# Kernel tuning notes

Measured on AMD Instinct MI355X. Metric: run time of the kernel, lower is better.

The kernel has to match this reference:

```python
import jax, jax.numpy as jnp
import numpy as np

B, S, V, H, NL, NH, FF, L = 32, 256, 30522, 768, 12, 12, 3072, 9
DH = H // NH
SCALE = 1.0 / float(np.sqrt(DH))

def _ln(x, g, b, eps=1e-12):
    mu = x.mean(-1, keepdims=True)
    var = ((x - mu) ** 2).mean(-1, keepdims=True)
    return (x - mu) * jax.lax.rsqrt(var + eps) * g + b

def _crf_nll(em, tags, mask, start, end, trans):
    # em: [B,S,L] log-softmaxed emissions; tags: [B,S] int; mask: [B,S] bool
    b, s, l = em.shape
    bi = jnp.arange(b)
    em_t = jnp.swapaxes(em, 0, 1)          # [S,B,L]
    tg_t = tags.T                           # [S,B]
    m_t = mask.T.astype(em.dtype)           # [S,B]
    # numerator: score of the gold path
    score0 = start[tags[:, 0]] + em[bi, 0, tags[:, 0]]
    def num_step(sc, xs):
        e, tg, tgp, m = xs
        return sc + m * (trans[tgp, tg] + e[bi, tg]), None
    num, _ = jax.lax.scan(num_step, score0, (em_t[1:], tg_t[1:], tg_t[:-1], m_t[1:]))
    seq_ends = mask.sum(1).astype(jnp.int32) - 1
    num = num + end[tags[bi, seq_ends]]
    # denominator: log partition via forward algorithm
    alpha0 = start[None, :] + em[:, 0]      # [B,L]
    def den_step(al, xs):
        e, m = xs
        new = jax.nn.logsumexp(al[:, :, None] + trans[None] + e[:, None, :], axis=1)
        return jnp.where(m[:, None] > 0, new, al), None
    alpha, _ = jax.lax.scan(den_step, alpha0, (em_t[1:], m_t[1:]))
    den = jax.nn.logsumexp(alpha + end[None, :], axis=1)
    return -(num - den).sum()   # torchcrf reduction='sum', negated in module

def _bert_crf_loss(token_ids, token_type_ids, attention_mask, y, p):
    b, s = token_ids.shape
    h = p['word_emb'][token_ids] + p['pos_emb'][:s][None] + p['type_emb'][token_type_ids]
    h = _ln(h, p['emb_ln_g'], p['emb_ln_b'])
    bias = (1.0 - attention_mask.astype(jnp.float32))[:, None, None, :] * -1e9
    def layer(hc, lp):
        Wq, bq, Wk, bk, Wv, bv, Wo, bo, g1, bln1, W1, b1, W2, b2, g2, bln2 = lp
        q = (hc @ Wq + bq).reshape(b, s, NH, DH)
        k = (hc @ Wk + bk).reshape(b, s, NH, DH)
        v = (hc @ Wv + bv).reshape(b, s, NH, DH)
        att = jnp.einsum('bqhd,bkhd->bhqk', q, k) * SCALE + bias
        att = jax.nn.softmax(att, axis=-1)
        ctx = jnp.einsum('bhqk,bkhd->bqhd', att, v).reshape(b, s, H)
        hc = _ln(hc + ctx @ Wo + bo, g1, bln1)
        ff = jax.nn.gelu(hc @ W1 + b1) @ W2 + b2
        hc = _ln(hc + ff, g2, bln2)
        return hc, None
    stacked = (p['Wq'], p['bq'], p['Wk'], p['bk'], p['Wv'], p['bv'], p['Wo'], p['bo'],
               p['ln1_g'], p['ln1_b'], p['W1'], p['b1'], p['W2'], p['b2'], p['ln2_g'], p['ln2_b'])
    h, _ = jax.lax.scan(layer, h, stacked)
    # dropout is identity in eval; fc has no bias; LogSoftmax over labels
    logits = jax.nn.log_softmax(h @ p['fc_w'], axis=-1)   # [B,S,L]
    return _crf_nll(logits, y, attention_mask.astype(bool), p['crf_start'], p['crf_end'], p['crf_trans'])

def setup_inputs() -> dict:
    key = jax.random.key(0)
    ks = iter(jax.random.split(key, 32))
    def nrm(shape, scale=0.02):
        return (jax.random.normal(next(ks), shape, jnp.float32) * scale)
    inp = dict(
        token_ids=jax.random.randint(next(ks), (B, S), 0, V),
        token_type_ids=jnp.zeros((B, S), jnp.int32),
        attention_mask=jnp.ones((B, S), jnp.int32),
        y=jax.random.randint(next(ks), (B, S), 0, L),
        word_emb=nrm((V, H)), pos_emb=nrm((S, H)), type_emb=nrm((2, H)),
        emb_ln_g=jnp.ones(H, jnp.float32), emb_ln_b=jnp.zeros(H, jnp.float32),
        Wq=nrm((NL, H, H)), bq=jnp.zeros((NL, H), jnp.float32),
        Wk=nrm((NL, H, H)), bk=jnp.zeros((NL, H), jnp.float32),
        Wv=nrm((NL, H, H)), bv=jnp.zeros((NL, H), jnp.float32),
        Wo=nrm((NL, H, H)), bo=jnp.zeros((NL, H), jnp.float32),
        ln1_g=jnp.ones((NL, H), jnp.float32), ln1_b=jnp.zeros((NL, H), jnp.float32),
        W1=nrm((NL, H, FF)), b1=jnp.zeros((NL, FF), jnp.float32),
        W2=nrm((NL, FF, H)), b2=jnp.zeros((NL, H), jnp.float32),
        ln2_g=jnp.ones((NL, H), jnp.float32), ln2_b=jnp.zeros((NL, H), jnp.float32),
        fc_w=nrm((H, L)),
        crf_start=nrm((L,), 0.1), crf_end=nrm((L,), 0.1), crf_trans=nrm((L, L), 0.1),
    )
    return inp

def reference(token_ids, token_type_ids, attention_mask, y, word_emb, pos_emb, type_emb,
              emb_ln_g, emb_ln_b, Wq, bq, Wk, bk, Wv, bv, Wo, bo, ln1_g, ln1_b,
              W1, b1, W2, b2, ln2_g, ln2_b, fc_w, crf_start, crf_end, crf_trans):
    p = dict(word_emb=word_emb, pos_emb=pos_emb, type_emb=type_emb,
             emb_ln_g=emb_ln_g, emb_ln_b=emb_ln_b, Wq=Wq, bq=bq, Wk=Wk, bk=bk,
             Wv=Wv, bv=bv, Wo=Wo, bo=bo, ln1_g=ln1_g, ln1_b=ln1_b,
             W1=W1, b1=b1, W2=W2, b2=b2, ln2_g=ln2_g, ln2_b=ln2_b,
             fc_w=fc_w, crf_start=crf_start, crf_end=crf_end, crf_trans=crf_trans)
    return _bert_crf_loss(token_ids, token_type_ids, attention_mask, y, p)
```

## Files before the change

### kernel.cpp

```cpp
#include <hip/hip_runtime.h>
#include <math.h>

typedef unsigned short ushortT;
typedef __attribute__((ext_vector_type(4))) float f32x4;
typedef __attribute__((ext_vector_type(4))) unsigned int u32x4;
typedef __attribute__((ext_vector_type(4))) unsigned short u16x4;
typedef __attribute__((ext_vector_type(4))) int i32x4;
typedef __attribute__((ext_vector_type(8))) __bf16 bf16x8;

namespace {
constexpr int S = 256;
constexpr int H = 768;
constexpr int NLAY = 12;
constexpr int NHD = 12;
constexpr int FF = 3072;
constexpr int LBL = 9;
constexpr int DH = 64;
constexpr int BATCH = 32;
constexpr int TOKENS = BATCH * S;
constexpr int QKVN = 3 * H;
constexpr float C2 = 0.18033688011112042f;

constexpr size_t HB_OFF  = 0;
constexpr size_t QB_OFF  = HB_OFF + (size_t)TOKENS*H/2;
constexpr size_t KB_OFF  = QB_OFF + (size_t)TOKENS*H/2;
constexpr size_t VT_OFF  = KB_OFF + (size_t)TOKENS*H/2;
constexpr size_t BIG_OFF = VT_OFF + (size_t)TOKENS*H/2;
constexpr size_t WTQ_OFF = BIG_OFF + (size_t)TOKENS*FF/2;
constexpr size_t WTO_OFF = WTQ_OFF + 3*(size_t)H*H/2;
constexpr size_t WT1_OFF = WTO_OFF + (size_t)H*H/2;
constexpr size_t WT2_OFF = WT1_OFF + (size_t)H*FF/2;
constexpr size_t EM_OFF  = WT2_OFF + (size_t)H*FF/2;
constexpr size_t PART_OFF= EM_OFF + (size_t)TOKENS*LBL;
constexpr size_t BQKV_OFF= PART_OFF + 64;
constexpr size_t WS_FLOATS = BQKV_OFF + (size_t)NLAY*QKVN;
}

__device__ __forceinline__ ushortT f2bf(float x) {
    unsigned u = __builtin_bit_cast(unsigned, x);
    u += 0x7fffu + ((u >> 16) & 1u);
    return (ushortT)(u >> 16);
}
__device__ __forceinline__ float bf2f(ushortT h) {
    unsigned u = ((unsigned)h) << 16;
    return __builtin_bit_cast(float, u);
}

__device__ __forceinline__ float exp2i(float x) {
    float r; asm("v_exp_f32 %0, %1" : "=v"(r) : "v"(x)); return r;
}
__device__ __forceinline__ float log2i(float x) {
    float r; asm("v_log_f32 %0, %1" : "=v"(r) : "v"(x)); return r;
}

__device__ __forceinline__ float gelu_tanh(float x) {
    float u = 0.7978845608028654f * (x + 0.044715f * x * x * x);
    float t = exp2i(-2.8853900817779268f * u);
    return x / (1.0f + t);
}

__device__ __forceinline__ f32x4 mfma16(u32x4 a, u32x4 b, f32x4 c) {
    return __builtin_amdgcn_mfma_f32_16x16x32_bf16(
        __builtin_bit_cast(bf16x8, a), __builtin_bit_cast(bf16x8, b), c, 0, 0, 0);
}

__device__ __forceinline__ void gload_lds16(const ushortT* g, ushortT* l) {
    __builtin_amdgcn_global_load_lds(
        (const __attribute__((address_space(1))) unsigned int*)g,
        (__attribute__((address_space(3))) unsigned int*)l,
        16, 0, 0);
}

template<int WM, int WN, int MODE>
__global__ __launch_bounds__(256) void gemm_mfma(
    const ushortT* __restrict__ A, int lda, long long sAo, long long sAi,
    const ushortT* __restrict__ Bt, int ldb, long long sBo, long long sBi,
    const float* __restrict__ bias,
    void* __restrict__ Cv, int ldc, long long sCo, long long sCi,
    int K, int innerN)
{
    constexpr int BM = WM * 64, BN = WN * 64;
    __shared__ __align__(16) ushortT As[3][BM * 32];
    __shared__ __align__(16) ushortT Bs[3][BN * 32];
    const int tid = threadIdx.x;
    const int wave = tid >> 6, lane = tid & 63;
    const int ob = blockIdx.z / innerN, ib = blockIdx.z - ob * innerN;

    int bxi = blockIdx.x, byi = blockIdx.y;
    if (gridDim.z == 1) {
        const int nwg = gridDim.x * gridDim.y;
        const int lin = byi * gridDim.x + bxi;
        const int cpx = nwg >> 3;
        const int sw = (lin & 7) * cpx + (lin >> 3);
        byi = sw / gridDim.x; bxi = sw - byi * gridDim.x;
    }
    const int bm = byi * BM, bn = bxi * BN;
    const ushortT* Ab = A + ob * sAo + ib * sAi + (size_t)bm * lda;
    const ushortT* Bb = Bt + ob * sBo + ib * sBi + (size_t)bn * ldb;
    const int wm = wave / WN, wn = wave - wm * WN;

    const int lrow = lane >> 2;
    const int lsw16 = ((lane & 3) ^ ((lrow >> 1) & 3)) * 8;
    const int rl = lane & 15;
    const int kg4 = (lane >> 4) << 2;
    const int ksw = ((lane >> 4) ^ ((rl >> 1) & 3)) << 3;

    f32x4 acc[4][4];
#pragma unroll
    for (int i = 0; i < 4; ++i)
#pragma unroll
        for (int j = 0; j < 4; ++j) acc[i][j] = (f32x4){0.f, 0.f, 0.f, 0.f};

    auto stage = [&](int buf, int k0) {
#pragma unroll
        for (int j = 0; j < WM; ++j) {
            int chunk = j * 4 + wave;
            gload_lds16(Ab + (size_t)(chunk * 16 + lrow) * lda + k0 + lsw16,
                        &As[buf][chunk * 512]);
        }
#pragma unroll
        for (int j = 0; j < WN; ++j) {
            int chunk = j * 4 + wave;
            gload_lds16(Bb + (size_t)(chunk * 16 + lrow) * ldb + k0 + lsw16,
                        &Bs[buf][chunk * 512]);
        }
    };

    const int nt = K >> 5;
    stage(0, 0);
    stage(1, ((nt > 1) ? 1 : 0) << 5);
    int cur = 0;
    for (int t = 0; t < nt; ++t) {
        if constexpr (WM + WN == 4)
            asm volatile("s_waitcnt vmcnt(4)" ::: "memory");
        else
            asm volatile("s_waitcnt vmcnt(5)" ::: "memory");
        __builtin_amdgcn_s_barrier();
        __builtin_amdgcn_sched_barrier(0);
        u32x4 a[4], b[4];
#pragma unroll
        for (int mf = 0; mf < 4; ++mf)
            a[mf] = *(const u32x4*)&As[cur][(wm * 64 + mf * 16 + rl) * 32 + ksw];
#pragma unroll
        for (int nf = 0; nf < 4; ++nf)
            b[nf] = *(const u32x4*)&Bs[cur][(wn * 64 + nf * 16 + rl) * 32 + ksw];
        {
            const int nx = (t + 2 < nt) ? t + 2 : nt - 1;
            int nb = cur + 2; if (nb >= 3) nb -= 3;
            stage(nb, nx << 5);
        }
#pragma unroll
        for (int mf = 0; mf < 4; ++mf)
#pragma unroll
            for (int nf = 0; nf < 4; ++nf)
                acc[mf][nf] = mfma16(a[mf], b[nf], acc[mf][nf]);
        cur = (cur + 1 == 3) ? 0 : cur + 1;
    }
    asm volatile("s_waitcnt vmcnt(0)" ::: "memory");

    ushortT* Ch = (ushortT*)Cv + ob * sCo + ib * sCi;
    if constexpr (MODE == 6) {
        __shared__ float red6[2][4][64];
        const int* mrow = (const int*)bias + ob * S;
        float mb[4];
#pragma unroll
        for (int nf = 0; nf < 4; ++nf)
            mb[nf] = mrow[bn + wn * 64 + nf * 16 + rl] ? 0.f : -8e9f;
        float pm[4][4];
#pragma unroll
        for (int mf = 0; mf < 4; ++mf)
#pragma unroll
            for (int r = 0; r < 4; ++r) pm[mf][r] = -1e30f;
#pragma unroll
        for (int mf = 0; mf < 4; ++mf)
#pragma unroll
            for (int nf = 0; nf < 4; ++nf)
#pragma unroll
                for (int r = 0; r < 4; ++r) {
                    acc[mf][nf][r] += mb[nf];
                    pm[mf][r] = fmaxf(pm[mf][r], acc[mf][nf][r]);
                }
#pragma unroll
        for (int mf = 0; mf < 4; ++mf)
#pragma unroll
            for (int r = 0; r < 4; ++r) {
                float v = pm[mf][r];
                v = fmaxf(v, __shfl_xor(v, 1));
                v = fmaxf(v, __shfl_xor(v, 2));
                v = fmaxf(v, __shfl_xor(v, 4));
                v = fmaxf(v, __shfl_xor(v, 8));
                pm[mf][r] = v;
            }
        if (rl == 0) {
#pragma unroll
            for (int mf = 0; mf < 4; ++mf)
#pragma unroll
                for (int r = 0; r < 4; ++r)
                    red6[0][wn][mf * 16 + kg4 + r] = pm[mf][r];
        }
        __syncthreads();
        float Mx[4][4];
#pragma unroll
        for (int mf = 0; mf < 4; ++mf)
#pragma unroll
            for (int r = 0; r < 4; ++r) {
                const int row = mf * 16 + kg4 + r;
                Mx[mf][r] = fmaxf(fmaxf(red6[0][0][row], red6[0][1][row]),
                                  fmaxf(red6[0][2][row], red6[0][3][row]));
            }
        float ps[4][4];
#pragma unroll
        for (int mf = 0; mf < 4; ++mf)
#pragma unroll
            for (int r = 0; r < 4; ++r) ps[mf][r] = 0.f;
#pragma unroll
        for (int mf = 0; mf < 4; ++mf)
#pragma unroll
            for (int nf = 0; nf < 4; ++nf)
#pragma unroll
                for (int r = 0; r < 4; ++r) {
                    float e = exp2i(C2 * (acc[mf][nf][r] - Mx[mf][r]));
                    acc[mf][nf][r] = e;
                    ps[mf][r] += e;
                }
#pragma unroll
        for (int mf = 0; mf < 4; ++mf)
#pragma unroll
            for (int r = 0; r < 4; ++r) {
                float v = ps[mf][r];
                v += __shfl_xor(v, 1);
                v += __shfl_xor(v, 2);
                v += __shfl_xor(v, 4);
                v += __shfl_xor(v, 8);
                ps[mf][r] = v;
            }
        if (rl == 0) {
#pragma unroll
            for (int mf = 0; mf < 4; ++mf)
#pragma unroll
                for (int r = 0; r < 4; ++r)
                    red6[1][wn][mf * 16 + kg4 + r] = ps[mf][r];
        }
        __syncthreads();
#pragma unroll
        for (int mf = 0; mf < 4; ++mf) {
            float inv[4];
#pragma unroll
            for (int r = 0; r < 4; ++r) {
                const int row = mf * 16 + kg4 + r;
                inv[r] = 1.0f / (red6[1][0][row] + red6[1][1][row] +
                                 red6[1][2][row] + red6[1][3][row]);
            }
#pragma unroll
            for (int nf = 0; nf < 4; ++nf) {
                const int gn = bn + wn * 64 + nf * 16 + rl;
                const int gm = bm + mf * 16 + kg4;
#pragma unroll
                for (int r = 0; r < 4; ++r)
                    Ch[(size_t)(gm + r) * ldc + gn] = f2bf(acc[mf][nf][r] * inv[r]);
            }
        }
    } else {
#pragma unroll
        for (int nf = 0; nf < 4; ++nf) {
            int gn = bn + wn * 64 + nf * 16 + rl;
            float bv = 0.f;
            if constexpr (MODE != 4) bv = bias[gn];
#pragma unroll
            for (int mf = 0; mf < 4; ++mf) {
                int gm = bm + wm * 64 + mf * 16 + kg4;
                if constexpr (MODE == 5) {
                    const int region = gn / H;
                    const int col = gn - region * H;
                    if (region < 2) {
                        ushortT* o = (ushortT*)Cv + (size_t)region * TOKENS * H;
#pragma unroll
                        for (int r = 0; r < 4; ++r)
                            o[(size_t)(gm + r) * H + col] = f2bf(acc[mf][nf][r] + bv);
                    } else {
                        u16x4 o;
#pragma unroll
                        for (int r = 0; r < 4; ++r) o[r] = f2bf(acc[mf][nf][r] + bv);
                        const int b_ = gm >> 8, s0 = gm & 255;
                        const int h_ = col >> 6, dh = col & 63;
                        *(u16x4*)((ushortT*)Cv + 2 * (size_t)TOKENS * H +
                                  (((size_t)(b_ * NHD + h_) * DH + dh) << 8) + s0) = o;
                    }
                } else {
#pragma unroll
                    for (int r = 0; r < 4; ++r) {
                        float x = acc[mf][nf][r] + bv;
                        if constexpr (MODE == 1) x = gelu_tanh(x);
                        Ch[(size_t)(gm + r) * ldc + gn] = f2bf(x);
                    }
                }
            }
        }
    }
}

__global__ __launch_bounds__(256) void transpose_all_k(
    const float* __restrict__ Wq, const float* __restrict__ Wk,
    const float* __restrict__ Wv, const float* __restrict__ Wo,
    const float* __restrict__ W1, const float* __restrict__ W2,
    ushortT* __restrict__ wtqkv, ushortT* __restrict__ wto,
    ushortT* __restrict__ wt1, ushortT* __restrict__ wt2)
{
    int idx = blockIdx.x;
    const float* W; ushortT* WT; int R, C, tr, tc;
    if (idx < 2304) {
        int mat = idx / 576, t = idx - mat * 576;
        tr = t / 24; tc = t - tr * 24; R = 768; C = 768;
        W = mat == 0 ? Wq : mat == 1 ? Wk : mat == 2 ? Wv : Wo;
        WT = mat < 3 ? wtqkv + (size_t)mat * 768 * 768 : wto;
    } else if (idx < 4608) {
        int t = idx - 2304; tr = t / 96; tc = t - tr * 96;
        R = 768; C = 3072; W = W1; WT = wt1;
    } else {
        int t = idx - 4608; tr = t / 24; tc = t - tr * 24;
        R = 3072; C = 768; W = W2; WT = wt2;
    }
    int r0 = tr * 32, c0 = tc * 32;
    __shared__ float tl[32][33];
    int trd = threadIdx.x >> 3;
    int tc4 = (threadIdx.x & 7) * 4;
    const float4 v = *(const float4*)(W + (size_t)(r0 + trd) * C + c0 + tc4);
    tl[trd][tc4 + 0] = v.x; tl[trd][tc4 + 1] = v.y;
    tl[trd][tc4 + 2] = v.z; tl[trd][tc4 + 3] = v.w;
    __syncthreads();
    u16x4 o;
#pragma unroll
    for (int q = 0; q < 4; ++q) o[q] = f2bf(tl[tc4 + q][trd]);
    *(u16x4*)(WT + (size_t)(c0 + trd) * R + r0 + tc4) = o;
}

__global__ __launch_bounds__(256) void pack_bias_k(
    const float* __restrict__ bq, const float* __restrict__ bk,
    const float* __restrict__ bv, float* __restrict__ out)
{
    int l = blockIdx.x / 3, r = blockIdx.x - (blockIdx.x / 3) * 3;
    const float* src = r == 0 ? bq : r == 1 ? bk : bv;
#pragma unroll
    for (int j = 0; j < 3; ++j) {
        int d = threadIdx.x + 256 * j;
        out[(size_t)l * QKVN + r * H + d] = src[(size_t)l * H + d];
    }
}

__global__ __launch_bounds__(256) void embed_ln_k(
    const int* __restrict__ ids, const int* __restrict__ tts,
    const float* __restrict__ wemb, const float* __restrict__ pemb,
    const float* __restrict__ temb, const float* __restrict__ g,
    const float* __restrict__ bp, ushortT* __restrict__ hb)
{
    const int tok = blockIdx.x * 4 + (threadIdx.x >> 6);
    const int lane = threadIdx.x & 63;
    const int d0 = lane * 12;
    const int spos = tok & (S - 1);
    const int id = ids[tok], tt = tts[tok];
    const float* wr = wemb + (size_t)id * H + d0;
    const float* pr = pemb + (size_t)spos * H + d0;
    const float* tr = temb + (size_t)tt * H + d0;
    float x[12]; float s = 0.f, ss = 0.f;
#pragma unroll
    for (int j = 0; j < 3; ++j) {
        float4 a = *(const float4*)(wr + j * 4);
        float4 b = *(const float4*)(pr + j * 4);
        float4 c = *(const float4*)(tr + j * 4);
        float v0 = a.x + b.x + c.x, v1 = a.y + b.y + c.y;
        float v2 = a.z + b.z + c.z, v3 = a.w + b.w + c.w;
        x[j*4+0] = v0; x[j*4+1] = v1; x[j*4+2] = v2; x[j*4+3] = v3;
        s += v0 + v1 + v2 + v3;
        ss += v0*v0 + v1*v1 + v2*v2 + v3*v3;
    }
#pragma unroll
    for (int m = 32; m; m >>= 1) { s += __shfl_xor(s, m); ss += __shfl_xor(ss, m); }
    float mu = s * (1.f / H);
    float var = ss * (1.f / H) - mu * mu;
    float rs = rsqrtf(var + 1e-12f);
#pragma unroll
    for (int j = 0; j < 3; ++j) {
        float4 gv = *(const float4*)(g + d0 + j * 4);
        float4 bv = *(const float4*)(bp + d0 + j * 4);
        u16x4 o;
        o[0] = f2bf((x[j*4+0] - mu) * rs * gv.x + bv.x);
        o[1] = f2bf((x[j*4+1] - mu) * rs * gv.y + bv.y);
        o[2] = f2bf((x[j*4+2] - mu) * rs * gv.z + bv.z);
        o[3] = f2bf((x[j*4+3] - mu) * rs * gv.w + bv.w);
        *(u16x4*)(hb + (size_t)tok * H + d0 + j * 4) = o;
    }
}

__global__ __launch_bounds__(256) void add_ln_k(
    ushortT* __restrict__ hb, const ushortT* __restrict__ add,
    const float* __restrict__ g, const float* __restrict__ bp)
{
    const int tok = blockIdx.x * 4 + (threadIdx.x >> 6);
    const int lane = threadIdx.x & 63;
    const int d0 = lane * 12;
    const size_t base = (size_t)tok * H + d0;
    float x[12]; float s = 0.f, ss = 0.f;
#pragma unroll
    for (int j = 0; j < 3; ++j) {
        u16x4 hv = *(const u16x4*)(hb + base + j * 4);
        u16x4 av = *(const u16x4*)(add + base + j * 4);
#pragma unroll
        for (int q = 0; q < 4; ++q) {
            float v = bf2f(hv[q]) + bf2f(av[q]);
            x[j*4+q] = v; s += v; ss += v * v;
        }
    }
#pragma unroll
    for (int m = 32; m; m >>= 1) { s += __shfl_xor(s, m); ss += __shfl_xor(ss, m); }
    float mu = s * (1.f / H);
    float var = ss * (1.f / H) - mu * mu;
    float rs = rsqrtf(var + 1e-12f);
#pragma unroll
    for (int j = 0; j < 3; ++j) {
        float4 gv = *(const float4*)(g + d0 + j * 4);
        float4 bv = *(const float4*)(bp + d0 + j * 4);
        u16x4 o;
        o[0] = f2bf((x[j*4+0] - mu) * rs * gv.x + bv.x);
        o[1] = f2bf((x[j*4+1] - mu) * rs * gv.y + bv.y);
        o[2] = f2bf((x[j*4+2] - mu) * rs * gv.z + bv.z);
        o[3] = f2bf((x[j*4+3] - mu) * rs * gv.w + bv.w);
        *(u16x4*)(hb + base + j * 4) = o;
    }
}

__global__ __launch_bounds__(256) void logits_k(
    const ushortT* __restrict__ hb, const float* __restrict__ fcw,
    float* __restrict__ em)
{
    int tok = blockIdx.x, tid = threadIdx.x;
    float p[LBL];
#pragma unroll
    for (int l = 0; l < LBL; ++l) p[l] = 0.f;
    const ushortT* hr = hb + (size_t)tok * H;
#pragma unroll
    for (int j = 0; j < 3; ++j) {
        int d = tid + 256 * j;
        float hv = bf2f(hr[d]);
        const float* fr = fcw + (size_t)d * LBL;
#pragma unroll
        for (int l = 0; l < LBL; ++l) p[l] = fmaf(hv, fr[l], p[l]);
    }
    __shared__ float ls[4][LBL];
    __shared__ float lg[LBL];
    __shared__ float lse;
#pragma unroll
    for (int l = 0; l < LBL; ++l) {
        float v = p[l];
#pragma unroll
        for (int m = 32; m; m >>= 1) v += __shfl_xor(v, m);
        if ((tid & 63) == 0) ls[tid >> 6][l] = v;
    }
    __syncthreads();
    if (tid < LBL) lg[tid] = ls[0][tid] + ls[1][tid] + ls[2][tid] + ls[3][tid];
    __syncthreads();
    if (tid == 0) {
        float mx = lg[0];
#pragma unroll
        for (int j = 1; j < LBL; ++j) mx = fmaxf(mx, lg[j]);
        float sm = 0.f;
#pragma unroll
        for (int j = 0; j < LBL; ++j) sm += expf(lg[j] - mx);
        lse = mx + logf(sm);
    }
    __syncthreads();
    if (tid < LBL) em[(size_t)tok * LBL + tid] = lg[tid] - lse;
}

__global__ __launch_bounds__(64) void crf_k(
    const float* __restrict__ em, const int* __restrict__ tags,
    const int* __restrict__ mask, const float* __restrict__ sp,
    const float* __restrict__ ep, const float* __restrict__ trans,
    float* __restrict__ partial)
{
    constexpr float LOG2E = 1.4426950408889634f;
    constexpr float LN2   = 0.6931471805599453f;
    int b = blockIdx.x, t = threadIdx.x;
    __shared__ float eml[S * LBL];
    __shared__ int mkl[S];
    const float* emb = em + (size_t)b * S * LBL;
    const int* tg = tags + (size_t)b * S;
    const int* mk = mask + (size_t)b * S;

    for (int i = t * 4; i < S * LBL; i += 256) {
        float4 v = *(const float4*)&emb[i];
        v.x *= LOG2E; v.y *= LOG2E; v.z *= LOG2E; v.w *= LOG2E;
        *(float4*)&eml[i] = v;
    }
    *(i32x4*)&mkl[t * 4] = *(const i32x4*)&mk[t * 4];

    int cnt = 0; float ns = 0.f;
    for (int i = t; i < S; i += 64) {
        int m = mk[i];
        cnt += (m != 0);
        if (i >= 1 && m)
            ns += trans[tg[i - 1] * LBL + tg[i]] + emb[(size_t)i * LBL + tg[i]];
    }
#pragma unroll
    for (int m = 32; m; m >>= 1) { cnt += __shfl_xor(cnt, m); ns += __shfl_xor(ns, m); }
    float num = ns + sp[tg[0]] + emb[tg[0]] + ep[tg[cnt - 1]];

    int tt = t < LBL ? t : 0;
    float trc2[LBL];
#pragma unroll
    for (int i = 0; i < LBL; ++i) trc2[i] = trans[i * LBL + tt] * LOG2E;

    __syncthreads();

    float alpha2 = (t < LBL) ? sp[t] * LOG2E + eml[t] : -1e30f;
    for (int step = 1; step < S; ++step) {
        float av[LBL];
#pragma unroll
        for (int i = 0; i < LBL; ++i) av[i] = __shfl(alpha2, i) + trc2[i];
        float mx = av[0];
#pragma unroll
        for (int i = 1; i < LBL; ++i) mx = fmaxf(mx, av[i]);
        float sm = 0.f;
#pragma unroll
        for (int i = 0; i < LBL; ++i) sm += exp2i(av[i] - mx);
        float na = mx + log2i(sm) + eml[step * LBL + tt];
        alpha2 = (mkl[step] && t < LBL) ? na : alpha2;
    }
    float z = (t < LBL) ? alpha2 + ep[t] * LOG2E : -1e30f;
    float mx = z;
#pragma unroll
    for (int m = 8; m; m >>= 1) mx = fmaxf(mx, __shfl_xor(mx, m));
    float sm = exp2i(z - mx);
#pragma unroll
    for (int m = 8; m; m >>= 1) sm += __shfl_xor(sm, m);
    if (t == 0) partial[b] = (mx + log2i(sm)) * LN2 - num;
}

__global__ void finalize_k(const float* __restrict__ partial, float* __restrict__ out) {
    float s = 0.f;
    for (int i = 0; i < BATCH; ++i) s += partial[i];
    out[0] = s;
}

__global__ void sentinel_k(float* out) { out[0] = -12345.0f; }

extern "C" void kernel_launch(void* const* d_in, const int* in_sizes, int n_in,
                              void* d_out, int out_size, void* d_ws, size_t ws_size,
                              hipStream_t stream) {
    (void)in_sizes; (void)n_in; (void)out_size;
    const int* token_ids  = (const int*)d_in[0];
    const int* token_type = (const int*)d_in[1];
    const int* amask      = (const int*)d_in[2];
    const int* y          = (const int*)d_in[3];
    const float* wemb = (const float*)d_in[4];
    const float* pemb = (const float*)d_in[5];
    const float* temb = (const float*)d_in[6];
    const float* eg   = (const float*)d_in[7];
    const float* eb   = (const float*)d_in[8];
    const float* Wq = (const float*)d_in[9];
    const float* bq = (const float*)d_in[10];
    const float* Wk = (const float*)d_in[11];
    const float* bk = (const float*)d_in[12];
    const float* Wv = (const float*)d_in[13];
    const float* bv = (const float*)d_in[14];
    const float* Wo = (const float*)d_in[15];
    const float* bo = (const float*)d_in[16];
    const float* ln1g = (const float*)d_in[17];
    const float* ln1b = (const float*)d_in[18];
    const float* W1 = (const float*)d_in[19];
    const float* b1 = (const float*)d_in[20];
    const float* W2 = (const float*)d_in[21];
    const float* b2 = (const float*)d_in[22];
    const float* ln2g = (const float*)d_in[23];
    const float* ln2b = (const float*)d_in[24];
    const float* fcw = (const float*)d_in[25];
    const float* crf_s = (const float*)d_in[26];
    const float* crf_e = (const float*)d_in[27];
    const float* crf_t = (const float*)d_in[28];

    if (ws_size < WS_FLOATS * sizeof(float)) {
        sentinel_k<<<1, 1, 0, stream>>>((float*)d_out);
        return;
    }

    float* ws = (float*)d_ws;
    ushortT* hb   = (ushortT*)(ws + HB_OFF);
    ushortT* qb   = (ushortT*)(ws + QB_OFF);
    ushortT* kb   = (ushortT*)(ws + KB_OFF);
    ushortT* vt   = (ushortT*)(ws + VT_OFF);
    ushortT* big  = (ushortT*)(ws + BIG_OFF);
    ushortT* wtq  = (ushortT*)(ws + WTQ_OFF);
    ushortT* wto  = (ushortT*)(ws + WTO_OFF);
    ushortT* wt1  = (ushortT*)(ws + WT1_OFF);
    ushortT* wt2  = (ushortT*)(ws + WT2_OFF);
    float*   embuf = ws + EM_OFF;
    float*   part  = ws + PART_OFF;
    float*   bqkv  = ws + BQKV_OFF;

    pack_bias_k<<<NLAY * 3, 256, 0, stream>>>(bq, bk, bv, bqkv);
    embed_ln_k<<<TOKENS / 4, 256, 0, stream>>>(token_ids, token_type, wemb, pemb,
                                               temb, eg, eb, hb);

    constexpr long long HH = (long long)H * H;
    constexpr long long HF = (long long)H * FF;
    constexpr long long TOKH = (long long)S * H;
    constexpr long long ATT_B = (long long)NHD * S * S;
    constexpr long long ATT_H = (long long)S * S;
    constexpr long long VT_B = (long long)NHD * DH * S;
    constexpr long long VT_H = (long long)DH * S;

    dim3 gQKV(QKVN / 128, TOKENS / 128, 1);
    dim3 gProj(H / 128, TOKENS / 128, 1);
    dim3 gFF1(FF / 128, TOKENS / 128, 1);
    dim3 gScores(1, S / 64, BATCH * NHD);
    dim3 gPV(1, 1, BATCH * NHD);

    for (int l = 0; l < NLAY; ++l) {
        transpose_all_k<<<6912, 256, 0, stream>>>(
            Wq + l * HH, Wk + l * HH, Wv + l * HH, Wo + l * HH,
            W1 + l * HF, W2 + l * HF, wtq, wto, wt1, wt2);

        gemm_mfma<2,2,5><<<gQKV, 256, 0, stream>>>(
            hb, H, 0, 0, wtq, H, 0, 0, bqkv + (size_t)l * QKVN,
            qb, H, 0, 0, H, 1);

        gemm_mfma<1,4,6><<<gScores, 256, 0, stream>>>(
            qb, H, TOKH, DH, kb, H, TOKH, DH, (const float*)amask,
            big, S, ATT_B, ATT_H, DH, NHD);

        gemm_mfma<4,1,4><<<gPV, 256, 0, stream>>>(
            big, S, ATT_B, ATT_H, vt, S, VT_B, VT_H, nullptr,
            qb, H, TOKH, DH, S, NHD);

        gemm_mfma<2,2,0><<<gProj, 256, 0, stream>>>(
            qb, H, 0, 0, wto, H, 0, 0, bo + l * H, kb, H, 0, 0, H, 1);

        add_ln_k<<<TOKENS / 4, 256, 0, stream>>>(hb, kb, ln1g + l * H, ln1b + l * H);

        gemm_mfma<2,2,1><<<gFF1, 256, 0, stream>>>(
            hb, H, 0, 0, wt1, H, 0, 0, b1 + (long long)l * FF, big, FF, 0, 0, H, 1);

        gemm_mfma<2,2,0><<<gProj, 256, 0, stream>>>(
            big, FF, 0, 0, wt2, FF, 0, 0, b2 + l * H, qb, H, 0, 0, FF, 1);

        add_ln_k<<<TOKENS / 4, 256, 0, stream>>>(hb, qb, ln2g + l * H, ln2b + l * H);
    }

    logits_k<<<TOKENS, 256, 0, stream>>>(hb, fcw, embuf);
    crf_k<<<BATCH, 64, 0, stream>>>(embuf, y, amask, crf_s, crf_e, crf_t, part);
    finalize_k<<<1, 1, 0, stream>>>(part, (float*)d_out);
}
```

Before: 3.073 ms.

## Add 128x256-tile GEMM kernel for dense projections with 8-way grid swizzle

Introduces a specialized gemm_wide kernel using 128x256 output tiles, where each wave computes a 64x128 sub-tile with a 4x8 MFMA fragment grid, a triple-buffered LDS pipeline, and XCD-aware block swizzling. The QKV, output projection, FF1 and FF2 GEMMs now use it, which raises arithmetic intensity per LDS load and halves the number of blocks. The risk is higher register pressure (128 accumulator floats per lane) and fewer blocks for the N=768 projections (3x64=192 blocks), which could underfill the 256 CUs.

New measurement: 4.304 ms. +40.0%, slower.

```diff
diff --git a/kernel.cpp b/kernel.cpp
--- a/kernel.cpp
+++ b/kernel.cpp
@@ -69,6 +69,124 @@
         (const __attribute__((address_space(1))) unsigned int*)g,
         (__attribute__((address_space(3))) unsigned int*)l,
         16, 0, 0);
+}
+
+template<int MODE>
+__global__ __launch_bounds__(256) void gemm_wide(
+    const ushortT* __restrict__ A, int lda,
+    const ushortT* __restrict__ Bt, int ldb,
+    const float* __restrict__ bias,
+    void* __restrict__ Cv, int ldc, int K)
+{
+    __shared__ __align__(16) ushortT As[3][128 * 32];
+    __shared__ __align__(16) ushortT Bs[3][256 * 32];
+    const int tid = threadIdx.x;
+    const int wave = tid >> 6, lane = tid & 63;
+
+    int bxi = blockIdx.x, byi = blockIdx.y;
+    {
+        const int nwg = gridDim.x * gridDim.y;
+        const int lin = byi * gridDim.x + bxi;
+        const int cpx = nwg >> 3;
+        const int sw = (lin & 7) * cpx + (lin >> 3);
+        byi = sw / gridDim.x; bxi = sw - byi * gridDim.x;
+    }
+    const int bm = byi * 128, bn = bxi * 256;
+    const ushortT* Ab = A + (size_t)bm * lda;
+    const ushortT* Bb = Bt + (size_t)bn * ldb;
+    const int wm = wave >> 1, wn = wave & 1;
+
+    const int lrow = lane >> 2;
+    const int lsw16 = ((lane & 3) ^ ((lrow >> 1) & 3)) * 8;
+    const int rl = lane & 15;
+    const int kg4 = (lane >> 4) << 2;
+    const int ksw = ((lane >> 4) ^ ((rl >> 1) & 3)) << 3;
+
+    f32x4 acc[4][8];
+#pragma unroll
+    for (int i = 0; i < 4; ++i)
+#pragma unroll
+        for (int j = 0; j < 8; ++j) acc[i][j] = (f32x4){0.f, 0.f, 0.f, 0.f};
+
+    auto stage = [&](int buf, int k0) {
+#pragma unroll
+        for (int j = 0; j < 2; ++j) {
+            int chunk = j * 4 + wave;
+            gload_lds16(Ab + (size_t)(chunk * 16 + lrow) * lda + k0 + lsw16,
+                        &As[buf][chunk * 512]);
+        }
+#pragma unroll
+        for (int j = 0; j < 4; ++j) {
+            int chunk = j * 4 + wave;
+            gload_lds16(Bb + (size_t)(chunk * 16 + lrow) * ldb + k0 + lsw16,
+                        &Bs[buf][chunk * 512]);
+        }
+    };
+
+    const int nt = K >> 5;
+    stage(0, 0);
+    stage(1, ((nt > 1) ? 1 : 0) << 5);
+    int cur = 0;
+    for (int t = 0; t < nt; ++t) {
+        asm volatile("s_waitcnt vmcnt(6)" ::: "memory");
+        __builtin_amdgcn_s_barrier();
+        __builtin_amdgcn_sched_barrier(0);
+        u32x4 a[4], b[8];
+#pragma unroll
+        for (int mf = 0; mf < 4; ++mf)
+            a[mf] = *(const u32x4*)&As[cur][(wm * 64 + mf * 16 + rl) * 32 + ksw];
+#pragma unroll
+        for (int nf = 0; nf < 8; ++nf)
+            b[nf] = *(const u32x4*)&Bs[cur][(wn * 128 + nf * 16 + rl) * 32 + ksw];
+        {
+            const int nx = (t + 2 < nt) ? t + 2 : nt - 1;
+            int nb = cur + 2; if (nb >= 3) nb -= 3;
+            stage(nb, nx << 5);
+        }
+#pragma unroll
+        for (int mf = 0; mf < 4; ++mf)
+#pragma unroll
+            for (int nf = 0; nf < 8; ++nf)
+                acc[mf][nf] = mfma16(a[mf], b[nf], acc[mf][nf]);
+        cur = (cur + 1 == 3) ? 0 : cur + 1;
+    }
+    asm volatile("s_waitcnt vmcnt(0)" ::: "memory");
+
+    ushortT* Ch = (ushortT*)Cv;
+#pragma unroll
+    for (int nf = 0; nf < 8; ++nf) {
+        const int gn = bn + wn * 128 + nf * 16 + rl;
+        const float bv = bias[gn];
+#pragma unroll
+        for (int mf = 0; mf < 4; ++mf) {
+            const int gm = bm + wm * 64 + mf * 16 + kg4;
+            if constexpr (MODE == 5) {
+                const int region = gn / H;
+                const int col = gn - region * H;
+                if (region < 2) {
+                    ushortT* o = (ushortT*)Cv + (size_t)region * TOKENS * H;
+#pragma unroll
+                    for (int r = 0; r < 4; ++r)
+                        o[(size_t)(gm + r) * H + col] = f2bf(acc[mf][nf][r] + bv);
+                } else {
+                    u16x4 o;
+#pragma unroll
+                    for (int r = 0; r < 4; ++r) o[r] = f2bf(acc[mf][nf][r] + bv);
+                    const int b_ = gm >> 8, s0 = gm & 255;
+                    const int h_ = col >> 6, dh = col & 63;
+                    *(u16x4*)((ushortT*)Cv + 2 * (size_t)TOKENS * H +
+                              (((size_t)(b_ * NHD + h_) * DH + dh) << 8) + s0) = o;
+                }
+            } else {
+#pragma unroll
+                for (int r = 0; r < 4; ++r) {
+                    float x = acc[mf][nf][r] + bv;
+                    if constexpr (MODE == 1) x = gelu_tanh(x);
+                    Ch[(size_t)(gm + r) * ldc + gn] = f2bf(x);
+                }
+            }
+        }
+    }
 }
 
 template<int WM, int WN, int MODE>
@@ -269,30 +387,11 @@
 #pragma unroll
             for (int mf = 0; mf < 4; ++mf) {
                 int gm = bm + wm * 64 + mf * 16 + kg4;
-                if constexpr (MODE == 5) {
-                    const int region = gn / H;
-                    const int col = gn - region * H;
-                    if (region < 2) {
-                        ushortT* o = (ushortT*)Cv + (size_t)region * TOKENS * H;
-#pragma unroll
-                        for (int r = 0; r < 4; ++r)
-                            o[(size_t)(gm + r) * H + col] = f2bf(acc[mf][nf][r] + bv);
-                    } else {
-                        u16x4 o;
-#pragma unroll
-                        for (int r = 0; r < 4; ++r) o[r] = f2bf(acc[mf][nf][r] + bv);
-                        const int b_ = gm >> 8, s0 = gm & 255;
-                        const int h_ = col >> 6, dh = col & 63;
-                        *(u16x4*)((ushortT*)Cv + 2 * (size_t)TOKENS * H +
-                                  (((size_t)(b_ * NHD + h_) * DH + dh) << 8) + s0) = o;
-                    }
-                } else {
-#pragma unroll
-                    for (int r = 0; r < 4; ++r) {
-                        float x = acc[mf][nf][r] + bv;
-                        if constexpr (MODE == 1) x = gelu_tanh(x);
-                        Ch[(size_t)(gm + r) * ldc + gn] = f2bf(x);
-                    }
+#pragma unroll
+                for (int r = 0; r < 4; ++r) {
+                    float x = acc[mf][nf][r] + bv;
+                    if constexpr (MODE == 1) x = gelu_tanh(x);
+                    Ch[(size_t)(gm + r) * ldc + gn] = f2bf(x);
                 }
             }
         }
@@ -608,9 +707,9 @@
     constexpr long long VT_B = (long long)NHD * DH * S;
     constexpr long long VT_H = (long long)DH * S;
 
-    dim3 gQKV(QKVN / 128, TOKENS / 128, 1);
-    dim3 gProj(H / 128, TOKENS / 128, 1);
-    dim3 gFF1(FF / 128, TOKENS / 128, 1);
+    dim3 gQKV(QKVN / 256, TOKENS / 128, 1);
+    dim3 gProj(H / 256, TOKENS / 128, 1);
+    dim3 gFF1(FF / 256, TOKENS / 128, 1);
     dim3 gScores(1, S / 64, BATCH * NHD);
     dim3 gPV(1, 1, BATCH * NHD);
 
@@ -619,9 +718,8 @@
             Wq + l * HH, Wk + l * HH, Wv + l * HH, Wo + l * HH,
             W1 + l * HF, W2 + l * HF, wtq, wto, wt1, wt2);
 
-        gemm_mfma<2,2,5><<<gQKV, 256, 0, stream>>>(
-            hb, H, 0, 0, wtq, H, 0, 0, bqkv + (size_t)l * QKVN,
-            qb, H, 0, 0, H, 1);
+        gemm_wide<5><<<gQKV, 256, 0, stream>>>(
+            hb, H, wtq, H, bqkv + (size_t)l * QKVN, qb, H, H);
 
         gemm_mfma<1,4,6><<<gScores, 256, 0, stream>>>(
             qb, H, TOKH, DH, kb, H, TOKH, DH, (const float*)amask,
@@ -631,16 +729,16 @@
             big, S, ATT_B, ATT_H, vt, S, VT_B, VT_H, nullptr,
             qb, H, TOKH, DH, S, NHD);
 
-        gemm_mfma<2,2,0><<<gProj, 256, 0, stream>>>(
-            qb, H, 0, 0, wto, H, 0, 0, bo + l * H, kb, H, 0, 0, H, 1);
+        gemm_wide<0><<<gProj, 256, 0, stream>>>(
+            qb, H, wto, H, bo + l * H, kb, H, H);
 
         add_ln_k<<<TOKENS / 4, 256, 0, stream>>>(hb, kb, ln1g + l * H, ln1b + l * H);
 
-        gemm_mfma<2,2,1><<<gFF1, 256, 0, stream>>>(
-            hb, H, 0, 0, wt1, H, 0, 0, b1 + (long long)l * FF, big, FF, 0, 0, H, 1);
-
-        gemm_mfma<2,2,0><<<gProj, 256, 0, stream>>>(
-            big, FF, 0, 0, wt2, FF, 0, 0, b2 + l * H, qb, H, 0, 0, FF, 1);
+        gemm_wide<1><<<gFF1, 256, 0, stream>>>(
+            hb, H, wt1, H, b1 + (long long)l * FF, big, FF, H);
+
+        gemm_wide<0><<<gProj, 256, 0, stream>>>(
+            big, FF, wt2, FF, b2 + l * H, qb, H, FF);
 
         add_ln_k<<<TOKENS / 4, 256, 0, stream>>>(hb, qb, ln2g + l * H, ln2b + l * H);
     }
```
